# Optimization experiments

Measured on AMD Instinct MI355X. Metric: run time of the kernel, lower is better.

The kernel has to match this reference:

```python
import jax, jax.numpy as jnp
import numpy as np

IN_DIM = 256
INNER = IN_DIM // 8  # 32


def setup_inputs() -> dict:
    key = jax.random.key(0)
    ks = jax.random.split(key, 9)
    B, C, W, H = 4, IN_DIM, 64, 64
    sc = 0.05
    return {
        "x": jax.random.normal(ks[0], (B, C, W, H), dtype=jnp.float32),
        "Wf": jax.random.normal(ks[1], (INNER, C), dtype=jnp.float32) * sc,
        "bf": jnp.zeros((INNER,), dtype=jnp.float32),
        "Wg": jax.random.normal(ks[2], (INNER, C), dtype=jnp.float32) * sc,
        "bg": jnp.zeros((INNER,), dtype=jnp.float32),
        "Wh": jax.random.normal(ks[3], (INNER, C), dtype=jnp.float32) * sc,
        "bh": jnp.zeros((INNER,), dtype=jnp.float32),
        "Wv": jax.random.normal(ks[4], (C, INNER), dtype=jnp.float32) * sc,
        "bv": jnp.zeros((C,), dtype=jnp.float32),
        "gamma": jnp.ones((1,), dtype=jnp.float32) * 0.5,  # nonzero so attention path matters
    }


def reference(x, Wf, bf, Wg, bg, Wh, bh, Wv, bv, gamma):
    B, C, W, H = x.shape
    N = W * H
    xf = x.reshape(B, C, N)
    # 1x1 convs == per-pixel linear projections
    f = jnp.einsum('kc,bcn->bkn', Wf, xf) + bf[None, :, None]  # [B, C/8, N]
    g = jnp.einsum('kc,bcn->bkn', Wg, xf) + bg[None, :, None]
    h = jnp.einsum('kc,bcn->bkn', Wh, xf) + bh[None, :, None]
    # s[b,n,m] = sum_k f[b,k,n] * g[b,k,m]  (f^T @ g)
    s = jnp.einsum('bkn,bkm->bnm', f, g)                      # [B, N, N]
    attn = jax.nn.softmax(s, axis=-1)                          # softmax over last dim
    attn_map = jnp.transpose(attn, (0, 2, 1))                  # returned map (permuted)
    # o_pre = h_x @ attn_map : o_pre[b,k,m] = sum_n h[b,k,n] * attn[b,m,n]
    o_pre = jnp.einsum('bkn,bmn->bkm', h, attn)                # [B, C/8, N]
    o = jnp.einsum('ck,bkn->bcn', Wv, o_pre) + bv[None, :, None]
    o = o.reshape(B, C, W, H)
    y = gamma.reshape(()) * o + x
    return (y, attn_map)
```

## Files before the change

kernel.cpp:

```cpp
#include <hip/hip_runtime.h>
#include <cstddef>
#include <cstdint>

#define NB     4
#define CDIM   256
#define KD     32
#define NPIX   4096
#define SSHIFT 20.0f

typedef __attribute__((ext_vector_type(8))) short  bfrag;
typedef __attribute__((ext_vector_type(4))) float  facc;

#define MFMA(a,b,c) __builtin_amdgcn_mfma_f32_16x16x32_bf16((a),(b),(c),0,0,0)

__device__ __forceinline__ unsigned short f2bf(float x) {
    union { float f; unsigned u; } v; v.f = x;
    unsigned u = v.u + 0x7fffu + ((v.u >> 16) & 1u);
    return (unsigned short)(u >> 16);
}
__device__ __forceinline__ float bf2f(unsigned short h) {
    union { float f; unsigned u; } v; v.u = ((unsigned)h) << 16;
    return v.f;
}

#define OFF_FA_HI (0)
#define OFF_FA_LO (1u<<20)
#define OFF_GB_HI (2u<<20)
#define OFF_GB_LO (3u<<20)
#define OFF_HB    (4u<<20)
#define OFF_WA_HI (5u<<20)
#define OFF_WA_LO ((5u<<20) + 65536)
#define OFF_OT    ((5u<<20) + 131072)
#define OFF_RCP   ((5u<<20) + 131072 + (2u<<20))

__global__ __launch_bounds__(256) void wt_kernel(const float* __restrict__ Wf,
                                                 const float* __restrict__ Wg,
                                                 const float* __restrict__ Wh,
                                                 unsigned short* __restrict__ WA_hi,
                                                 unsigned short* __restrict__ WA_lo)
{
    int t = blockIdx.x * 256 + threadIdx.x;
    if (t >= 48 * 64) return;
    int tile = t >> 6, lane = t & 63;
    int rt = tile >> 3, cc = tile & 7;
    int q = lane >> 4, c15 = lane & 15;
    int row = rt * 16 + c15;
    const float* W = (row < 32) ? (Wf + (size_t)row * CDIM)
                   : (row < 64) ? (Wg + (size_t)(row - 32) * CDIM)
                                : (Wh + (size_t)(row - 64) * CDIM);
    int cb = cc * 32 + q * 8;
    bfrag vh, vl;
#pragma unroll
    for (int j = 0; j < 8; ++j) {
        float xv = W[cb + j];
        unsigned short h = f2bf(xv);
        vh[j] = (short)h;
        vl[j] = (short)f2bf(xv - bf2f(h));
    }
    *(bfrag*)(WA_hi + (size_t)t * 8) = vh;
    *(bfrag*)(WA_lo + (size_t)t * 8) = vl;
}

__global__ __launch_bounds__(256) void proj_kernel(const float* __restrict__ x,
                                                   const unsigned short* __restrict__ WA_hi,
                                                   const unsigned short* __restrict__ WA_lo,
                                                   const float* __restrict__ bfv,
                                                   const float* __restrict__ bgv,
                                                   const float* __restrict__ bhv,
                                                   unsigned short* __restrict__ fA_hi,
                                                   unsigned short* __restrict__ fA_lo,
                                                   unsigned short* __restrict__ gB_hi,
                                                   unsigned short* __restrict__ gB_lo,
                                                   unsigned short* __restrict__ hB)
{
    __shared__ float xs[32][65];
    __shared__ float os[96][65];
    __shared__ float bias_s[96];

    const int b  = blockIdx.y;
    const int n0 = blockIdx.x * 64;
    const int tid = threadIdx.x;
    const int w = tid >> 6, lane = tid & 63, q = lane >> 4, c15 = lane & 15;

    if (tid < 96)
        bias_s[tid] = (tid < 32) ? bfv[tid] : (tid < 64 ? bgv[tid - 32] : bhv[tid - 64]);

    facc acc[6];
#pragma unroll
    for (int rt = 0; rt < 6; ++rt) acc[rt] = (facc){0.f, 0.f, 0.f, 0.f};

    const float* xb = x + (size_t)b * CDIM * NPIX + n0;
    const int cr = tid >> 3, nb = (tid & 7) * 8;

    for (int cc = 0; cc < 8; ++cc) {
        const float* src = xb + (size_t)(cc * 32 + cr) * NPIX + nb;
        float4 va = *(const float4*)src;
        float4 vb = *(const float4*)(src + 4);
        __syncthreads();
        *(float4*)&xs[cr][nb]     = va;
        *(float4*)&xs[cr][nb + 4] = vb;
        __syncthreads();

        bfrag xh, xl;
#pragma unroll
        for (int j = 0; j < 8; ++j) {
            float xv = xs[q * 8 + j][w * 16 + c15];
            unsigned short h = f2bf(xv);
            xh[j] = (short)h;
            xl[j] = (short)f2bf(xv - bf2f(h));
        }
#pragma unroll
        for (int rt = 0; rt < 6; ++rt) {
            size_t wo = ((size_t)(rt * 8 + cc) * 64 + lane) * 8;
            bfrag wh = *(const bfrag*)(WA_hi + wo);
            bfrag wl = *(const bfrag*)(WA_lo + wo);
            acc[rt] = MFMA(wh, xh, acc[rt]);
            acc[rt] = MFMA(wh, xl, acc[rt]);
            acc[rt] = MFMA(wl, xh, acc[rt]);
        }
    }

#pragma unroll
    for (int rt = 0; rt < 6; ++rt)
#pragma unroll
        for (int i = 0; i < 4; ++i) {
            int row = rt * 16 + q * 4 + i;
            os[row][w * 16 + c15] = acc[rt][i] + bias_s[row];
        }
    __syncthreads();

    {
        bfrag vh, vl;
#pragma unroll
        for (int j = 0; j < 8; ++j) {
            float v = os[q * 8 + j][w * 16 + c15];
            unsigned short h = f2bf(v);
            vh[j] = (short)h; vl[j] = (short)f2bf(v - bf2f(h));
        }
        size_t o = ((size_t)(b * 256 + (n0 >> 4) + w) * 64 + lane) * 8;
        *(bfrag*)(fA_hi + o) = vh;
        *(bfrag*)(fA_lo + o) = vl;
#pragma unroll
        for (int j = 0; j < 8; ++j) {
            float v = os[32 + q * 8 + j][w * 16 + c15];
            unsigned short h = f2bf(v);
            vh[j] = (short)h; vl[j] = (short)f2bf(v - bf2f(h));
        }
        *(bfrag*)(gB_hi + o) = vh;
        *(bfrag*)(gB_lo + o) = vl;
        int mcl = w >> 1, kt = w & 1;
        bfrag hv;
#pragma unroll
        for (int j = 0; j < 8; ++j) {
            int p = q * 8 + j;
            int mp = (p & 1) * 16 + (p >> 1);
            float v = os[64 + kt * 16 + c15][mcl * 32 + mp];
            hv[j] = (short)f2bf(v);
        }
        size_t oh = ((size_t)((b * 128 + (n0 >> 5) + mcl) * 2 + kt) * 64 + lane) * 8;
        *(bfrag*)(hB + oh) = hv;
    }
}

__global__ __launch_bounds__(256) void attn_kernel(const unsigned short* __restrict__ fA_hi,
                                                   const unsigned short* __restrict__ fA_lo,
                                                   const unsigned short* __restrict__ gB_hi,
                                                   const unsigned short* __restrict__ gB_lo,
                                                   const unsigned short* __restrict__ hB,
                                                   float* __restrict__ rcp_g,
                                                   float* __restrict__ oT)
{
    __shared__ unsigned short Pst[4][16 * 40];
    __shared__ float red[4][64][8];
    __shared__ float sums_l[4][16];
    __shared__ float rcp_l[16];

    const int b  = blockIdx.y;
    const int r0 = blockIdx.x * 16;
    const int tid = threadIdx.x;
    const int w = tid >> 6, lane = tid & 63, q = lane >> 4, c15 = lane & 15;

    const size_t fo = ((size_t)(b * 256 + (r0 >> 4)) * 64 + lane) * 8;
    const bfrag fh = *(const bfrag*)(fA_hi + fo);
    const bfrag fl = *(const bfrag*)(fA_lo + fo);

    facc o0 = (facc){0.f,0.f,0.f,0.f}, o1 = (facc){0.f,0.f,0.f,0.f};
    float sum[4] = {0.f, 0.f, 0.f, 0.f};
    unsigned short* P = &Pst[w][0];

    const int ch0 = w * 32, ch1 = ch0 + 32;

    for (int mc = ch0; mc < ch1; ++mc) {
        size_t go = ((size_t)(b * 256 + 2 * mc) * 64 + lane) * 8;
        bfrag g0h = *(const bfrag*)(gB_hi + go);
        bfrag g1h = *(const bfrag*)(gB_hi + go + 512);
        bfrag g0l = *(const bfrag*)(gB_lo + go);
        bfrag g1l = *(const bfrag*)(gB_lo + go + 512);
        size_t ho = ((size_t)(b * 128 + mc) * 2 * 64 + lane) * 8;
        bfrag h0 = *(const bfrag*)(hB + ho);
        bfrag h1 = *(const bfrag*)(hB + ho + 512);

        facc s0 = (facc){0.f,0.f,0.f,0.f}, s1 = (facc){0.f,0.f,0.f,0.f};
        s0 = MFMA(fh, g0h, s0); s0 = MFMA(fh, g0l, s0); s0 = MFMA(fl, g0h, s0);
        s1 = MFMA(fh, g1h, s1); s1 = MFMA(fh, g1l, s1); s1 = MFMA(fl, g1h, s1);

        float e0[4], e1[4];
#pragma unroll
        for (int i = 0; i < 4; ++i) {
            e0[i] = __expf(s0[i] - SSHIFT);
            e1[i] = __expf(s1[i] - SSHIFT);
            sum[i] += e0[i] + e1[i];
        }
#pragma unroll
        for (int i = 0; i < 4; ++i) {
            unsigned pr = (unsigned)f2bf(e0[i]) | ((unsigned)f2bf(e1[i]) << 16);
            *(unsigned*)&P[(4 * q + i) * 40 + 2 * c15] = pr;
        }
        bfrag pA = *(const bfrag*)&P[c15 * 40 + q * 8];
        o0 = MFMA(pA, h0, o0);
        o1 = MFMA(pA, h1, o1);
    }

#pragma unroll
    for (int m = 1; m < 16; m <<= 1)
#pragma unroll
        for (int i = 0; i < 4; ++i) sum[i] += __shfl_xor(sum[i], m);
    if (c15 == 0) {
#pragma unroll
        for (int i = 0; i < 4; ++i) sums_l[w][4 * q + i] = sum[i];
    }
    *(facc*)&red[w][lane][0] = o0;
    *(facc*)&red[w][lane][4] = o1;
    __syncthreads();
    if (tid < 16) {
        float rv = 1.0f / (sums_l[0][tid] + sums_l[1][tid] + sums_l[2][tid] + sums_l[3][tid]);
        rcp_l[tid] = rv;
        rcp_g[(size_t)b * NPIX + r0 + tid] = rv;
    }
    __syncthreads();

    if (w == 0) {
        facc a = (facc){0.f,0.f,0.f,0.f}, bb = (facc){0.f,0.f,0.f,0.f};
#pragma unroll
        for (int ww = 0; ww < 4; ++ww) {
            a  += *(const facc*)&red[ww][lane][0];
            bb += *(const facc*)&red[ww][lane][4];
        }
#pragma unroll
        for (int i = 0; i < 4; ++i) {
            int r = 4 * q + i;
            float rc = rcp_l[r];
            oT[((size_t)(b * NPIX + r0 + r)) * KD + c15]      = a[i] * rc;
            oT[((size_t)(b * NPIX + r0 + r)) * KD + 16 + c15] = bb[i] * rc;
        }
    }
}

__global__ __launch_bounds__(256) void attn2_kernel(const unsigned short* __restrict__ fA_hi,
                                                    const unsigned short* __restrict__ fA_lo,
                                                    const unsigned short* __restrict__ gB_hi,
                                                    const unsigned short* __restrict__ gB_lo,
                                                    const float* __restrict__ rcp_g,
                                                    float* __restrict__ am)
{
    const int b   = blockIdx.y;
    const int mt  = blockIdx.x;
    const int tid = threadIdx.x;
    const int w = tid >> 6, lane = tid & 63, q = lane >> 4, c15 = lane & 15;

    const size_t ga = ((size_t)(b * 256 + mt) * 64 + lane) * 8;
    const bfrag a_hi = *(const bfrag*)(gB_hi + ga);
    const bfrag a_lo = *(const bfrag*)(gB_lo + ga);

    const int m0 = mt * 16 + q * 4;
    float* amrow = am + (size_t)b * NPIX * NPIX + (size_t)m0 * NPIX;
    const float* rcp_b = rcp_g + (size_t)b * NPIX;

#pragma unroll 2
    for (int t = 0; t < 64; ++t) {
        const int nt = w * 64 + t;
        const size_t fo = ((size_t)(b * 256 + nt) * 64 + lane) * 8;
        bfrag b_hi = *(const bfrag*)(fA_hi + fo);
        bfrag b_lo = *(const bfrag*)(fA_lo + fo);

        facc s = (facc){0.f,0.f,0.f,0.f};
        s = MFMA(a_hi, b_hi, s);
        s = MFMA(a_hi, b_lo, s);
        s = MFMA(a_lo, b_hi, s);

        const int n = nt * 16 + c15;
        const float rc = rcp_b[n];
#pragma unroll
        for (int i = 0; i < 4; ++i)
            amrow[(size_t)i * NPIX + n] = __expf(s[i] - SSHIFT) * rc;
    }
}

__global__ __launch_bounds__(256) void out_kernel(const float* __restrict__ x,
                                                  const float* __restrict__ oT,
                                                  const float* __restrict__ Wv,
                                                  const float* __restrict__ bv,
                                                  const float* __restrict__ gamma,
                                                  float* __restrict__ y)
{
    __shared__ float wv_s[CDIM * KD];
    const int b  = blockIdx.y;
    const int tid = threadIdx.x;
    const int n = blockIdx.x * 64 + (tid & 63);
    const int cg = tid >> 6;

    for (int i = tid * 4; i < CDIM * KD; i += 1024)
        *(float4*)&wv_s[i] = *(const float4*)&Wv[i];

    float op[KD];
    {
        const float4* src = (const float4*)&oT[((size_t)(b * NPIX + n)) * KD];
#pragma unroll
        for (int qq = 0; qq < 8; ++qq) {
            float4 v = src[qq];
            op[qq * 4 + 0] = v.x; op[qq * 4 + 1] = v.y;
            op[qq * 4 + 2] = v.z; op[qq * 4 + 3] = v.w;
        }
    }
    __syncthreads();
    const float gm = gamma[0];

    for (int c = cg * 64; c < cg * 64 + 64; ++c) {
        float a = 0.f;
#pragma unroll
        for (int k4 = 0; k4 < 8; ++k4) {
            float4 wv4 = *(const float4*)&wv_s[c * KD + k4 * 4];
            a = fmaf(wv4.x, op[k4 * 4 + 0], a);
            a = fmaf(wv4.y, op[k4 * 4 + 1], a);
            a = fmaf(wv4.z, op[k4 * 4 + 2], a);
            a = fmaf(wv4.w, op[k4 * 4 + 3], a);
        }
        size_t idx = ((size_t)(b * CDIM + c)) * NPIX + n;
        y[idx] = fmaf(gm, a + bv[c], x[idx]);
    }
}

extern "C" void kernel_launch(void* const* d_in, const int* in_sizes, int n_in,
                              void* d_out, int out_size, void* d_ws, size_t ws_size,
                              hipStream_t stream)
{
    const float* x     = (const float*)d_in[0];
    const float* Wf    = (const float*)d_in[1];
    const float* bfv   = (const float*)d_in[2];
    const float* Wg    = (const float*)d_in[3];
    const float* bgv   = (const float*)d_in[4];
    const float* Wh    = (const float*)d_in[5];
    const float* bhv   = (const float*)d_in[6];
    const float* Wv    = (const float*)d_in[7];
    const float* bv    = (const float*)d_in[8];
    const float* gamma = (const float*)d_in[9];

    char* ws = (char*)d_ws;
    unsigned short* fA_hi = (unsigned short*)(ws + OFF_FA_HI);
    unsigned short* fA_lo = (unsigned short*)(ws + OFF_FA_LO);
    unsigned short* gB_hi = (unsigned short*)(ws + OFF_GB_HI);
    unsigned short* gB_lo = (unsigned short*)(ws + OFF_GB_LO);
    unsigned short* hB    = (unsigned short*)(ws + OFF_HB);
    unsigned short* WA_hi = (unsigned short*)(ws + OFF_WA_HI);
    unsigned short* WA_lo = (unsigned short*)(ws + OFF_WA_LO);
    float*          oT    = (float*)(ws + OFF_OT);
    float*          rcp_g = (float*)(ws + OFF_RCP);

    float* y  = (float*)d_out;
    float* am = (float*)d_out + (size_t)NB * CDIM * NPIX;

    hipLaunchKernelGGL(wt_kernel, dim3(12), dim3(256), 0, stream, Wf, Wg, Wh, WA_hi, WA_lo);
    hipLaunchKernelGGL(proj_kernel, dim3(NPIX / 64, NB), dim3(256), 0, stream,
                       x, WA_hi, WA_lo, bfv, bgv, bhv, fA_hi, fA_lo, gB_hi, gB_lo, hB);
    hipLaunchKernelGGL(attn_kernel, dim3(NPIX / 16, NB), dim3(256), 0, stream,
                       fA_hi, fA_lo, gB_hi, gB_lo, hB, rcp_g, oT);
    hipLaunchKernelGGL(attn2_kernel, dim3(NPIX / 16, NB), dim3(256), 0, stream,
                       fA_hi, fA_lo, gB_hi, gB_lo, rcp_g, am);
    hipLaunchKernelGGL(out_kernel, dim3(NPIX / 64, NB), dim3(256), 0, stream,
                       x, oT, Wv, bv, gamma, y);
}
```

Baseline: 412.3 us.

## Merge attention-map and output kernels into one launch with nontemporal stores

Combines the attention-map writer and the output projection into a single tail kernel, with blocks dispatched by blockIdx.x to one role or the other, so the two independent stages overlap and one launch is saved. Each attention-map block now handles two 16-row m tiles, reusing every loaded f fragment for both. The large attention-map and y writes use nontemporal stores to avoid polluting the cache. In exchange every block reserves the 32KB shared buffer even when only the output blocks use it, which can lower occupancy for the attention-map blocks, and halving their count may reduce parallelism.

```diff
diff --git a/kernel.cpp b/kernel.cpp
--- a/kernel.cpp
+++ b/kernel.cpp
@@ -256,87 +256,97 @@
     }
 }
 
-__global__ __launch_bounds__(256) void attn2_kernel(const unsigned short* __restrict__ fA_hi,
-                                                    const unsigned short* __restrict__ fA_lo,
-                                                    const unsigned short* __restrict__ gB_hi,
-                                                    const unsigned short* __restrict__ gB_lo,
-                                                    const float* __restrict__ rcp_g,
-                                                    float* __restrict__ am)
-{
+__global__ __launch_bounds__(256) void tail_kernel(const unsigned short* __restrict__ fA_hi,
+                                                   const unsigned short* __restrict__ fA_lo,
+                                                   const unsigned short* __restrict__ gB_hi,
+                                                   const unsigned short* __restrict__ gB_lo,
+                                                   const float* __restrict__ rcp_g,
+                                                   float* __restrict__ am,
+                                                   const float* __restrict__ x,
+                                                   const float* __restrict__ oT,
+                                                   const float* __restrict__ Wv,
+                                                   const float* __restrict__ bv,
+                                                   const float* __restrict__ gamma,
+                                                   float* __restrict__ y)
+{
+    __shared__ float wv_s[CDIM * KD];
+
     const int b   = blockIdx.y;
-    const int mt  = blockIdx.x;
+    const int bx  = blockIdx.x;
     const int tid = threadIdx.x;
-    const int w = tid >> 6, lane = tid & 63, q = lane >> 4, c15 = lane & 15;
-
-    const size_t ga = ((size_t)(b * 256 + mt) * 64 + lane) * 8;
-    const bfrag a_hi = *(const bfrag*)(gB_hi + ga);
-    const bfrag a_lo = *(const bfrag*)(gB_lo + ga);
-
-    const int m0 = mt * 16 + q * 4;
-    float* amrow = am + (size_t)b * NPIX * NPIX + (size_t)m0 * NPIX;
-    const float* rcp_b = rcp_g + (size_t)b * NPIX;
+
+    if (bx < 128) {
+        const int w = tid >> 6, lane = tid & 63, q = lane >> 4, c15 = lane & 15;
+
+        const size_t ga = ((size_t)(b * 256 + 2 * bx) * 64 + lane) * 8;
+        const bfrag a0h = *(const bfrag*)(gB_hi + ga);
+        const bfrag a0l = *(const bfrag*)(gB_lo + ga);
+        const bfrag a1h = *(const bfrag*)(gB_hi + ga + 512);
+        const bfrag a1l = *(const bfrag*)(gB_lo + ga + 512);
+
+        const int m0 = bx * 32 + q * 4;
+        float* amrow = am + (size_t)b * NPIX * NPIX + (size_t)m0 * NPIX;
+        const float* rcp_b = rcp_g + (size_t)b * NPIX;
 
 #pragma unroll 2
-    for (int t = 0; t < 64; ++t) {
-        const int nt = w * 64 + t;
-        const size_t fo = ((size_t)(b * 256 + nt) * 64 + lane) * 8;
-        bfrag b_hi = *(const bfrag*)(fA_hi + fo);
-        bfrag b_lo = *(const bfrag*)(fA_lo + fo);
-
-        facc s = (facc){0.f,0.f,0.f,0.f};
-        s = MFMA(a_hi, b_hi, s);
-        s = MFMA(a_hi, b_lo, s);
-        s = MFMA(a_lo, b_hi, s);
-
-        const int n = nt * 16 + c15;
-        const float rc = rcp_b[n];
-#pragma unroll
-        for (int i = 0; i < 4; ++i)
-            amrow[(size_t)i * NPIX + n] = __expf(s[i] - SSHIFT) * rc;
-    }
-}
-
-__global__ __launch_bounds__(256) void out_kernel(const float* __restrict__ x,
-                                                  const float* __restrict__ oT,
-                                                  const float* __restrict__ Wv,
-                                                  const float* __restrict__ bv,
-                                                  const float* __restrict__ gamma,
-                                                  float* __restrict__ y)
-{
-    __shared__ float wv_s[CDIM * KD];
-    const int b  = blockIdx.y;
-    const int tid = threadIdx.x;
-    const int n = blockIdx.x * 64 + (tid & 63);
-    const int cg = tid >> 6;
-
-    for (int i = tid * 4; i < CDIM * KD; i += 1024)
-        *(float4*)&wv_s[i] = *(const float4*)&Wv[i];
-
-    float op[KD];
-    {
-        const float4* src = (const float4*)&oT[((size_t)(b * NPIX + n)) * KD];
-#pragma unroll
-        for (int qq = 0; qq < 8; ++qq) {
-            float4 v = src[qq];
-            op[qq * 4 + 0] = v.x; op[qq * 4 + 1] = v.y;
-            op[qq * 4 + 2] = v.z; op[qq * 4 + 3] = v.w;
-        }
-    }
-    __syncthreads();
-    const float gm = gamma[0];
-
-    for (int c = cg * 64; c < cg * 64 + 64; ++c) {
-        float a = 0.f;
-#pragma unroll
-        for (int k4 = 0; k4 < 8; ++k4) {
-            float4 wv4 = *(const float4*)&wv_s[c * KD + k4 * 4];
-            a = fmaf(wv4.x, op[k4 * 4 + 0], a);
-            a = fmaf(wv4.y, op[k4 * 4 + 1], a);
-            a = fmaf(wv4.z, op[k4 * 4 + 2], a);
-            a = fmaf(wv4.w, op[k4 * 4 + 3], a);
-        }
-        size_t idx = ((size_t)(b * CDIM + c)) * NPIX + n;
-        y[idx] = fmaf(gm, a + bv[c], x[idx]);
+        for (int t = 0; t < 64; ++t) {
+            const int nt = w * 64 + t;
+            const size_t fo = ((size_t)(b * 256 + nt) * 64 + lane) * 8;
+            bfrag b_hi = *(const bfrag*)(fA_hi + fo);
+            bfrag b_lo = *(const bfrag*)(fA_lo + fo);
+
+            facc s0 = (facc){0.f,0.f,0.f,0.f};
+            s0 = MFMA(a0h, b_hi, s0);
+            s0 = MFMA(a0h, b_lo, s0);
+            s0 = MFMA(a0l, b_hi, s0);
+            facc s1 = (facc){0.f,0.f,0.f,0.f};
+            s1 = MFMA(a1h, b_hi, s1);
+            s1 = MFMA(a1h, b_lo, s1);
+            s1 = MFMA(a1l, b_hi, s1);
+
+            const int n = nt * 16 + c15;
+            const float rc = rcp_b[n];
+#pragma unroll
+            for (int i = 0; i < 4; ++i) {
+                __builtin_nontemporal_store(__expf(s0[i] - SSHIFT) * rc,
+                                            &amrow[(size_t)i * NPIX + n]);
+                __builtin_nontemporal_store(__expf(s1[i] - SSHIFT) * rc,
+                                            &amrow[(size_t)(16 + i) * NPIX + n]);
+            }
+        }
+    } else {
+        const int n = (bx - 128) * 64 + (tid & 63);
+        const int cg = tid >> 6;
+
+        for (int i = tid * 4; i < CDIM * KD; i += 1024)
+            *(float4*)&wv_s[i] = *(const float4*)&Wv[i];
+
+        float op[KD];
+        {
+            const float4* src = (const float4*)&oT[((size_t)(b * NPIX + n)) * KD];
+#pragma unroll
+            for (int qq = 0; qq < 8; ++qq) {
+                float4 v = src[qq];
+                op[qq * 4 + 0] = v.x; op[qq * 4 + 1] = v.y;
+                op[qq * 4 + 2] = v.z; op[qq * 4 + 3] = v.w;
+            }
+        }
+        __syncthreads();
+        const float gm = gamma[0];
+
+        for (int c = cg * 64; c < cg * 64 + 64; ++c) {
+            float a = 0.f;
+#pragma unroll
+            for (int k4 = 0; k4 < 8; ++k4) {
+                float4 wv4 = *(const float4*)&wv_s[c * KD + k4 * 4];
+                a = fmaf(wv4.x, op[k4 * 4 + 0], a);
+                a = fmaf(wv4.y, op[k4 * 4 + 1], a);
+                a = fmaf(wv4.z, op[k4 * 4 + 2], a);
+                a = fmaf(wv4.w, op[k4 * 4 + 3], a);
+            }
+            size_t idx = ((size_t)(b * CDIM + c)) * NPIX + n;
+            __builtin_nontemporal_store(fmaf(gm, a + bv[c], x[idx]), &y[idx]);
+        }
     }
 }
 
@@ -374,8 +384,6 @@
                        x, WA_hi, WA_lo, bfv, bgv, bhv, fA_hi, fA_lo, gB_hi, gB_lo, hB);
     hipLaunchKernelGGL(attn_kernel, dim3(NPIX / 16, NB), dim3(256), 0, stream,
                        fA_hi, fA_lo, gB_hi, gB_lo, hB, rcp_g, oT);
-    hipLaunchKernelGGL(attn2_kernel, dim3(NPIX / 16, NB), dim3(256), 0, stream,
-                       fA_hi, fA_lo, gB_hi, gB_lo, rcp_g, am);
-    hipLaunchKernelGGL(out_kernel, dim3(NPIX / 64, NB), dim3(256), 0, stream,
-                       x, oT, Wv, bv, gamma, y);
-}
+    hipLaunchKernelGGL(tail_kernel, dim3(128 + NPIX / 64, NB), dim3(256), 0, stream,
+                       fA_hi, fA_lo, gB_hi, gB_lo, rcp_g, am, x, oT, Wv, bv, gamma, y);
+}
```

Result: slower. 428.8 us (+4.0%).

## Fuse pipeline into cooperative persistent kernel and fold output projection into attention

Applied to the files above, without the earlier changes.

Merges the weight prep, projection, attention and attention-map stages into one cooperative kernel with grid-wide syncs, which removes several kernel launches. The output 1x1 conv and residual are folded into the attention kernel through a shared-memory oT tile, so the global oT buffer and its round trip go away. Attention-map writes now use nontemporal stores. In exchange, the large shared allocation in the mega kernel limits occupancy, the grid syncs add barrier cost, and if the cooperative launch fails the code falls back to separate kernels.

```diff
diff --git a/kernel.cpp b/kernel.cpp
--- a/kernel.cpp
+++ b/kernel.cpp
@@ -1,6 +1,9 @@
 #include <hip/hip_runtime.h>
+#include <hip/hip_cooperative_groups.h>
 #include <cstddef>
 #include <cstdint>
+
+namespace cg = cooperative_groups;
 
 #define NB     4
 #define CDIM   256
@@ -30,17 +33,24 @@
 #define OFF_HB    (4u<<20)
 #define OFF_WA_HI (5u<<20)
 #define OFF_WA_LO ((5u<<20) + 65536)
-#define OFF_OT    ((5u<<20) + 131072)
 #define OFF_RCP   ((5u<<20) + 131072 + (2u<<20))
 
-__global__ __launch_bounds__(256) void wt_kernel(const float* __restrict__ Wf,
-                                                 const float* __restrict__ Wg,
-                                                 const float* __restrict__ Wh,
-                                                 unsigned short* __restrict__ WA_hi,
-                                                 unsigned short* __restrict__ WA_lo)
-{
-    int t = blockIdx.x * 256 + threadIdx.x;
-    if (t >= 48 * 64) return;
+#define SM_PROJ_BYTES 33664
+#define SM_XS   0
+#define SM_OS   8320
+#define SM_BIAS 33280
+#define SM_PST  0
+#define SM_RED  5120
+#define SM_SUMS 13312
+#define SM_RCPL 13568
+#define SM_OTS  13632
+#define SM_ATTN_BYTES 15680
+
+__device__ __forceinline__ void wt_body(int t,
+        const float* __restrict__ Wf, const float* __restrict__ Wg,
+        const float* __restrict__ Wh,
+        unsigned short* __restrict__ WA_hi, unsigned short* __restrict__ WA_lo)
+{
     int tile = t >> 6, lane = t & 63;
     int rt = tile >> 3, cc = tile & 7;
     int q = lane >> 4, c15 = lane & 15;
@@ -61,25 +71,19 @@
     *(bfrag*)(WA_lo + (size_t)t * 8) = vl;
 }
 
-__global__ __launch_bounds__(256) void proj_kernel(const float* __restrict__ x,
-                                                   const unsigned short* __restrict__ WA_hi,
-                                                   const unsigned short* __restrict__ WA_lo,
-                                                   const float* __restrict__ bfv,
-                                                   const float* __restrict__ bgv,
-                                                   const float* __restrict__ bhv,
-                                                   unsigned short* __restrict__ fA_hi,
-                                                   unsigned short* __restrict__ fA_lo,
-                                                   unsigned short* __restrict__ gB_hi,
-                                                   unsigned short* __restrict__ gB_lo,
-                                                   unsigned short* __restrict__ hB)
-{
-    __shared__ float xs[32][65];
-    __shared__ float os[96][65];
-    __shared__ float bias_s[96];
-
-    const int b  = blockIdx.y;
-    const int n0 = blockIdx.x * 64;
-    const int tid = threadIdx.x;
+__device__ __forceinline__ void proj_body(char* smem, int b, int n0, int tid,
+        const float* __restrict__ x,
+        const unsigned short* __restrict__ WA_hi, const unsigned short* __restrict__ WA_lo,
+        const float* __restrict__ bfv, const float* __restrict__ bgv,
+        const float* __restrict__ bhv,
+        unsigned short* __restrict__ fA_hi, unsigned short* __restrict__ fA_lo,
+        unsigned short* __restrict__ gB_hi, unsigned short* __restrict__ gB_lo,
+        unsigned short* __restrict__ hB)
+{
+    float* xs     = (float*)(smem + SM_XS);
+    float* os     = (float*)(smem + SM_OS);
+    float* bias_s = (float*)(smem + SM_BIAS);
+
     const int w = tid >> 6, lane = tid & 63, q = lane >> 4, c15 = lane & 15;
 
     if (tid < 96)
@@ -97,14 +101,14 @@
         float4 va = *(const float4*)src;
         float4 vb = *(const float4*)(src + 4);
         __syncthreads();
-        *(float4*)&xs[cr][nb]     = va;
-        *(float4*)&xs[cr][nb + 4] = vb;
+        *(float4*)&xs[cr * 65 + nb]     = va;
+        *(float4*)&xs[cr * 65 + nb + 4] = vb;
         __syncthreads();
 
         bfrag xh, xl;
 #pragma unroll
         for (int j = 0; j < 8; ++j) {
-            float xv = xs[q * 8 + j][w * 16 + c15];
+            float xv = xs[(q * 8 + j) * 65 + w * 16 + c15];
             unsigned short h = f2bf(xv);
             xh[j] = (short)h;
             xl[j] = (short)f2bf(xv - bf2f(h));
@@ -125,7 +129,7 @@
 #pragma unroll
         for (int i = 0; i < 4; ++i) {
             int row = rt * 16 + q * 4 + i;
-            os[row][w * 16 + c15] = acc[rt][i] + bias_s[row];
+            os[row * 65 + w * 16 + c15] = acc[rt][i] + bias_s[row];
         }
     __syncthreads();
 
@@ -133,7 +137,7 @@
         bfrag vh, vl;
 #pragma unroll
         for (int j = 0; j < 8; ++j) {
-            float v = os[q * 8 + j][w * 16 + c15];
+            float v = os[(q * 8 + j) * 65 + w * 16 + c15];
             unsigned short h = f2bf(v);
             vh[j] = (short)h; vl[j] = (short)f2bf(v - bf2f(h));
         }
@@ -142,7 +146,7 @@
         *(bfrag*)(fA_lo + o) = vl;
 #pragma unroll
         for (int j = 0; j < 8; ++j) {
-            float v = os[32 + q * 8 + j][w * 16 + c15];
+            float v = os[(32 + q * 8 + j) * 65 + w * 16 + c15];
             unsigned short h = f2bf(v);
             vh[j] = (short)h; vl[j] = (short)f2bf(v - bf2f(h));
         }
@@ -154,7 +158,7 @@
         for (int j = 0; j < 8; ++j) {
             int p = q * 8 + j;
             int mp = (p & 1) * 16 + (p >> 1);
-            float v = os[64 + kt * 16 + c15][mcl * 32 + mp];
+            float v = os[(64 + kt * 16 + c15) * 65 + mcl * 32 + mp];
             hv[j] = (short)f2bf(v);
         }
         size_t oh = ((size_t)((b * 128 + (n0 >> 5) + mcl) * 2 + kt) * 64 + lane) * 8;
@@ -162,22 +166,20 @@
     }
 }
 
-__global__ __launch_bounds__(256) void attn_kernel(const unsigned short* __restrict__ fA_hi,
-                                                   const unsigned short* __restrict__ fA_lo,
-                                                   const unsigned short* __restrict__ gB_hi,
-                                                   const unsigned short* __restrict__ gB_lo,
-                                                   const unsigned short* __restrict__ hB,
-                                                   float* __restrict__ rcp_g,
-                                                   float* __restrict__ oT)
-{
-    __shared__ unsigned short Pst[4][16 * 40];
-    __shared__ float red[4][64][8];
-    __shared__ float sums_l[4][16];
-    __shared__ float rcp_l[16];
-
-    const int b  = blockIdx.y;
-    const int r0 = blockIdx.x * 16;
-    const int tid = threadIdx.x;
+__device__ __forceinline__ void attn1_body(char* smem, int b, int r0, int tid,
+        const unsigned short* __restrict__ fA_hi, const unsigned short* __restrict__ fA_lo,
+        const unsigned short* __restrict__ gB_hi, const unsigned short* __restrict__ gB_lo,
+        const unsigned short* __restrict__ hB, float* __restrict__ rcp_g,
+        const float* __restrict__ x, const float* __restrict__ Wv,
+        const float* __restrict__ bv, const float* __restrict__ gamma,
+        float* __restrict__ y)
+{
+    unsigned short* Pst = (unsigned short*)(smem + SM_PST);
+    float* red    = (float*)(smem + SM_RED);
+    float* sums_l = (float*)(smem + SM_SUMS);
+    float* rcp_l  = (float*)(smem + SM_RCPL);
+    float* oTs    = (float*)(smem + SM_OTS);
+
     const int w = tid >> 6, lane = tid & 63, q = lane >> 4, c15 = lane & 15;
 
     const size_t fo = ((size_t)(b * 256 + (r0 >> 4)) * 64 + lane) * 8;
@@ -186,7 +188,7 @@
 
     facc o0 = (facc){0.f,0.f,0.f,0.f}, o1 = (facc){0.f,0.f,0.f,0.f};
     float sum[4] = {0.f, 0.f, 0.f, 0.f};
-    unsigned short* P = &Pst[w][0];
+    unsigned short* P = Pst + w * 640;
 
     const int ch0 = w * 32, ch1 = ch0 + 32;
 
@@ -227,13 +229,13 @@
         for (int i = 0; i < 4; ++i) sum[i] += __shfl_xor(sum[i], m);
     if (c15 == 0) {
 #pragma unroll
-        for (int i = 0; i < 4; ++i) sums_l[w][4 * q + i] = sum[i];
-    }
-    *(facc*)&red[w][lane][0] = o0;
-    *(facc*)&red[w][lane][4] = o1;
+        for (int i = 0; i < 4; ++i) sums_l[w * 16 + 4 * q + i] = sum[i];
+    }
+    *(facc*)&red[(w * 64 + lane) * 8]     = o0;
+    *(facc*)&red[(w * 64 + lane) * 8 + 4] = o1;
     __syncthreads();
     if (tid < 16) {
-        float rv = 1.0f / (sums_l[0][tid] + sums_l[1][tid] + sums_l[2][tid] + sums_l[3][tid]);
+        float rv = 1.0f / (sums_l[tid] + sums_l[16 + tid] + sums_l[32 + tid] + sums_l[48 + tid]);
         rcp_l[tid] = rv;
         rcp_g[(size_t)b * NPIX + r0 + tid] = rv;
     }
@@ -243,29 +245,56 @@
         facc a = (facc){0.f,0.f,0.f,0.f}, bb = (facc){0.f,0.f,0.f,0.f};
 #pragma unroll
         for (int ww = 0; ww < 4; ++ww) {
-            a  += *(const facc*)&red[ww][lane][0];
-            bb += *(const facc*)&red[ww][lane][4];
+            a  += *(const facc*)&red[(ww * 64 + lane) * 8];
+            bb += *(const facc*)&red[(ww * 64 + lane) * 8 + 4];
         }
 #pragma unroll
         for (int i = 0; i < 4; ++i) {
             int r = 4 * q + i;
             float rc = rcp_l[r];
-            oT[((size_t)(b * NPIX + r0 + r)) * KD + c15]      = a[i] * rc;
-            oT[((size_t)(b * NPIX + r0 + r)) * KD + 16 + c15] = bb[i] * rc;
-        }
-    }
-}
-
-__global__ __launch_bounds__(256) void attn2_kernel(const unsigned short* __restrict__ fA_hi,
-                                                    const unsigned short* __restrict__ fA_lo,
-                                                    const unsigned short* __restrict__ gB_hi,
-                                                    const unsigned short* __restrict__ gB_lo,
-                                                    const float* __restrict__ rcp_g,
-                                                    float* __restrict__ am)
-{
-    const int b   = blockIdx.y;
-    const int mt  = blockIdx.x;
-    const int tid = threadIdx.x;
+            oTs[r * 32 + c15]      = a[i] * rc;
+            oTs[r * 32 + 16 + c15] = bb[i] * rc;
+        }
+    }
+    __syncthreads();
+
+    {
+        const int c = w * 64 + lane;
+        const float gm = gamma[0];
+        const float4* wvp = (const float4*)(Wv + (size_t)c * KD);
+        float4 wv[8];
+#pragma unroll
+        for (int k4 = 0; k4 < 8; ++k4) wv[k4] = wvp[k4];
+        const float bvc = bv[c];
+        const size_t base = ((size_t)(b * CDIM + c)) * NPIX + r0;
+#pragma unroll
+        for (int nn = 0; nn < 16; nn += 4) {
+            float4 xv = *(const float4*)(x + base + nn);
+            float4 yo;
+#pragma unroll
+            for (int j = 0; j < 4; ++j) {
+                const float4* ot = (const float4*)(oTs + (nn + j) * 32);
+                float a = 0.f;
+#pragma unroll
+                for (int k4 = 0; k4 < 8; ++k4) {
+                    float4 o4 = ot[k4];
+                    a = fmaf(wv[k4].x, o4.x, a);
+                    a = fmaf(wv[k4].y, o4.y, a);
+                    a = fmaf(wv[k4].z, o4.z, a);
+                    a = fmaf(wv[k4].w, o4.w, a);
+                }
+                ((float*)&yo)[j] = fmaf(gm, a + bvc, ((float*)&xv)[j]);
+            }
+            *(float4*)(y + base + nn) = yo;
+        }
+    }
+}
+
+__device__ __forceinline__ void attn2_body(int b, int mt, int tid,
+        const unsigned short* __restrict__ fA_hi, const unsigned short* __restrict__ fA_lo,
+        const unsigned short* __restrict__ gB_hi, const unsigned short* __restrict__ gB_lo,
+        const float* __restrict__ rcp_g, float* __restrict__ am)
+{
     const int w = tid >> 6, lane = tid & 63, q = lane >> 4, c15 = lane & 15;
 
     const size_t ga = ((size_t)(b * 256 + mt) * 64 + lane) * 8;
@@ -292,52 +321,91 @@
         const float rc = rcp_b[n];
 #pragma unroll
         for (int i = 0; i < 4; ++i)
-            amrow[(size_t)i * NPIX + n] = __expf(s[i] - SSHIFT) * rc;
-    }
-}
-
-__global__ __launch_bounds__(256) void out_kernel(const float* __restrict__ x,
-                                                  const float* __restrict__ oT,
-                                                  const float* __restrict__ Wv,
-                                                  const float* __restrict__ bv,
-                                                  const float* __restrict__ gamma,
-                                                  float* __restrict__ y)
-{
-    __shared__ float wv_s[CDIM * KD];
-    const int b  = blockIdx.y;
+            __builtin_nontemporal_store(__expf(s[i] - SSHIFT) * rc,
+                                        &amrow[(size_t)i * NPIX + n]);
+    }
+}
+
+__global__ __launch_bounds__(256, 4) void mega_kernel(
+        const float* __restrict__ x,
+        const float* __restrict__ Wf, const float* __restrict__ bfv,
+        const float* __restrict__ Wg, const float* __restrict__ bgv,
+        const float* __restrict__ Wh, const float* __restrict__ bhv,
+        const float* __restrict__ Wv, const float* __restrict__ bv,
+        const float* __restrict__ gamma,
+        unsigned short* __restrict__ fA_hi, unsigned short* __restrict__ fA_lo,
+        unsigned short* __restrict__ gB_hi, unsigned short* __restrict__ gB_lo,
+        unsigned short* __restrict__ hB,
+        unsigned short* __restrict__ WA_hi, unsigned short* __restrict__ WA_lo,
+        float* __restrict__ rcp_g, float* __restrict__ am, float* __restrict__ y)
+{
+    cg::grid_group grid = cg::this_grid();
+    __shared__ __align__(16) char smem[SM_PROJ_BYTES];
+
+    const int gid = blockIdx.x;
     const int tid = threadIdx.x;
-    const int n = blockIdx.x * 64 + (tid & 63);
-    const int cg = tid >> 6;
-
-    for (int i = tid * 4; i < CDIM * KD; i += 1024)
-        *(float4*)&wv_s[i] = *(const float4*)&Wv[i];
-
-    float op[KD];
-    {
-        const float4* src = (const float4*)&oT[((size_t)(b * NPIX + n)) * KD];
-#pragma unroll
-        for (int qq = 0; qq < 8; ++qq) {
-            float4 v = src[qq];
-            op[qq * 4 + 0] = v.x; op[qq * 4 + 1] = v.y;
-            op[qq * 4 + 2] = v.z; op[qq * 4 + 3] = v.w;
-        }
-    }
-    __syncthreads();
-    const float gm = gamma[0];
-
-    for (int c = cg * 64; c < cg * 64 + 64; ++c) {
-        float a = 0.f;
-#pragma unroll
-        for (int k4 = 0; k4 < 8; ++k4) {
-            float4 wv4 = *(const float4*)&wv_s[c * KD + k4 * 4];
-            a = fmaf(wv4.x, op[k4 * 4 + 0], a);
-            a = fmaf(wv4.y, op[k4 * 4 + 1], a);
-            a = fmaf(wv4.z, op[k4 * 4 + 2], a);
-            a = fmaf(wv4.w, op[k4 * 4 + 3], a);
-        }
-        size_t idx = ((size_t)(b * CDIM + c)) * NPIX + n;
-        y[idx] = fmaf(gm, a + bv[c], x[idx]);
-    }
+
+    if (gid < 12) {
+        int t = gid * 256 + tid;
+        if (t < 48 * 64)
+            wt_body(t, Wf, Wg, Wh, WA_hi, WA_lo);
+    }
+    grid.sync();
+
+    if (gid < 256)
+        proj_body(smem, gid >> 6, (gid & 63) * 64, tid,
+                  x, WA_hi, WA_lo, bfv, bgv, bhv, fA_hi, fA_lo, gB_hi, gB_lo, hB);
+    grid.sync();
+
+    attn1_body(smem, gid >> 8, (gid & 255) * 16, tid,
+               fA_hi, fA_lo, gB_hi, gB_lo, hB, rcp_g, x, Wv, bv, gamma, y);
+    grid.sync();
+
+    attn2_body(gid >> 8, gid & 255, tid, fA_hi, fA_lo, gB_hi, gB_lo, rcp_g, am);
+}
+
+__global__ __launch_bounds__(256) void wt_kernel(const float* __restrict__ Wf,
+                                                 const float* __restrict__ Wg,
+                                                 const float* __restrict__ Wh,
+                                                 unsigned short* __restrict__ WA_hi,
+                                                 unsigned short* __restrict__ WA_lo)
+{
+    int t = blockIdx.x * 256 + threadIdx.x;
+    if (t < 48 * 64) wt_body(t, Wf, Wg, Wh, WA_hi, WA_lo);
+}
+
+__global__ __launch_bounds__(256) void proj_kernel(const float* __restrict__ x,
+        const unsigned short* __restrict__ WA_hi, const unsigned short* __restrict__ WA_lo,
+        const float* __restrict__ bfv, const float* __restrict__ bgv,
+        const float* __restrict__ bhv,
+        unsigned short* __restrict__ fA_hi, unsigned short* __restrict__ fA_lo,
+        unsigned short* __restrict__ gB_hi, unsigned short* __restrict__ gB_lo,
+        unsigned short* __restrict__ hB)
+{
+    __shared__ __align__(16) char smem[SM_PROJ_BYTES];
+    proj_body(smem, blockIdx.y, blockIdx.x * 64, threadIdx.x,
+              x, WA_hi, WA_lo, bfv, bgv, bhv, fA_hi, fA_lo, gB_hi, gB_lo, hB);
+}
+
+__global__ __launch_bounds__(256) void attn1_kernel(
+        const unsigned short* __restrict__ fA_hi, const unsigned short* __restrict__ fA_lo,
+        const unsigned short* __restrict__ gB_hi, const unsigned short* __restrict__ gB_lo,
+        const unsigned short* __restrict__ hB, float* __restrict__ rcp_g,
+        const float* __restrict__ x, const float* __restrict__ Wv,
+        const float* __restrict__ bv, const float* __restrict__ gamma,
+        float* __restrict__ y)
+{
+    __shared__ __align__(16) char smem[SM_ATTN_BYTES];
+    attn1_body(smem, blockIdx.y, blockIdx.x * 16, threadIdx.x,
+               fA_hi, fA_lo, gB_hi, gB_lo, hB, rcp_g, x, Wv, bv, gamma, y);
+}
+
+__global__ __launch_bounds__(256) void attn2_kernel(
+        const unsigned short* __restrict__ fA_hi, const unsigned short* __restrict__ fA_lo,
+        const unsigned short* __restrict__ gB_hi, const unsigned short* __restrict__ gB_lo,
+        const float* __restrict__ rcp_g, float* __restrict__ am)
+{
+    attn2_body(blockIdx.y, blockIdx.x, threadIdx.x, fA_hi, fA_lo, gB_hi, gB_lo, rcp_g, am);
 }
 
 extern "C" void kernel_launch(void* const* d_in, const int* in_sizes, int n_in,
@@ -363,19 +431,26 @@
     unsigned short* hB    = (unsigned short*)(ws + OFF_HB);
     unsigned short* WA_hi = (unsigned short*)(ws + OFF_WA_HI);
     unsigned short* WA_lo = (unsigned short*)(ws + OFF_WA_LO);
-    float*          oT    = (float*)(ws + OFF_OT);
     float*          rcp_g = (float*)(ws + OFF_RCP);
 
     float* y  = (float*)d_out;
     float* am = (float*)d_out + (size_t)NB * CDIM * NPIX;
 
-    hipLaunchKernelGGL(wt_kernel, dim3(12), dim3(256), 0, stream, Wf, Wg, Wh, WA_hi, WA_lo);
-    hipLaunchKernelGGL(proj_kernel, dim3(NPIX / 64, NB), dim3(256), 0, stream,
-                       x, WA_hi, WA_lo, bfv, bgv, bhv, fA_hi, fA_lo, gB_hi, gB_lo, hB);
-    hipLaunchKernelGGL(attn_kernel, dim3(NPIX / 16, NB), dim3(256), 0, stream,
-                       fA_hi, fA_lo, gB_hi, gB_lo, hB, rcp_g, oT);
-    hipLaunchKernelGGL(attn2_kernel, dim3(NPIX / 16, NB), dim3(256), 0, stream,
-                       fA_hi, fA_lo, gB_hi, gB_lo, rcp_g, am);
-    hipLaunchKernelGGL(out_kernel, dim3(NPIX / 64, NB), dim3(256), 0, stream,
-                       x, oT, Wv, bv, gamma, y);
-}
+    void* args[] = { &x, &Wf, &bfv, &Wg, &bgv, &Wh, &bhv, &Wv, &bv, &gamma,
+                     &fA_hi, &fA_lo, &gB_hi, &gB_lo, &hB, &WA_hi, &WA_lo,
+                     &rcp_g, &am, &y };
+    hipError_t e = hipLaunchCooperativeKernel(
+        reinterpret_cast<const void*>(&mega_kernel),
+        dim3(1024), dim3(256), args, 0u, stream);
+
+    if (e != hipSuccess) {
+        hipLaunchKernelGGL(wt_kernel, dim3(12), dim3(256), 0, stream,
+                           Wf, Wg, Wh, WA_hi, WA_lo);
+        hipLaunchKernelGGL(proj_kernel, dim3(NPIX / 64, NB), dim3(256), 0, stream,
+                           x, WA_hi, WA_lo, bfv, bgv, bhv, fA_hi, fA_lo, gB_hi, gB_lo, hB);
+        hipLaunchKernelGGL(attn1_kernel, dim3(NPIX / 16, NB), dim3(256), 0, stream,
+                           fA_hi, fA_lo, gB_hi, gB_lo, hB, rcp_g, x, Wv, bv, gamma, y);
+        hipLaunchKernelGGL(attn2_kernel, dim3(NPIX / 16, NB), dim3(256), 0, stream,
+                           fA_hi, fA_lo, gB_hi, gB_lo, rcp_g, am);
+    }
+}
```

New measurement: 691.8 us. 67.8% more time.

## Prefetch next-iteration fragments and remap blocks for XCD-local batch placement

Applied to the files above, without the earlier changes.

Both attention kernels now load the next iteration's g/h (or f) fragments and the reciprocal before computing the current step, a software-pipelining step meant to hide global load latency behind MFMA and exp work. The grids are flattened to 1D, and block ids are remapped so that consecutive ids, which are dealt round-robin across the 8 XCDs, land so that each XCD works on a single batch. This keeps that batch's g/h/f data in one XCD's L2. The cost is extra registers for the prefetched fragments, which may lower occupancy.

```diff
diff --git a/kernel.cpp b/kernel.cpp
--- a/kernel.cpp
+++ b/kernel.cpp
@@ -162,6 +162,28 @@
     }
 }
 
+#define ATTN1_STEP(G0H,G1H,G0L,G1L,H0,H1)                                       \
+    {                                                                           \
+        facc s0 = (facc){0.f,0.f,0.f,0.f}, s1 = (facc){0.f,0.f,0.f,0.f};        \
+        s0 = MFMA(fh, G0H, s0); s0 = MFMA(fh, G0L, s0); s0 = MFMA(fl, G0H, s0); \
+        s1 = MFMA(fh, G1H, s1); s1 = MFMA(fh, G1L, s1); s1 = MFMA(fl, G1H, s1); \
+        float e0[4], e1[4];                                                     \
+        _Pragma("unroll")                                                       \
+        for (int i = 0; i < 4; ++i) {                                           \
+            e0[i] = __expf(s0[i] - SSHIFT);                                     \
+            e1[i] = __expf(s1[i] - SSHIFT);                                     \
+            sum[i] += e0[i] + e1[i];                                            \
+        }                                                                       \
+        _Pragma("unroll")                                                       \
+        for (int i = 0; i < 4; ++i) {                                           \
+            unsigned pr = (unsigned)f2bf(e0[i]) | ((unsigned)f2bf(e1[i]) << 16);\
+            *(unsigned*)&P[(4 * q + i) * 40 + 2 * c15] = pr;                    \
+        }                                                                       \
+        bfrag pA = *(const bfrag*)&P[c15 * 40 + q * 8];                         \
+        o0 = MFMA(pA, H0, o0);                                                  \
+        o1 = MFMA(pA, H1, o1);                                                  \
+    }
+
 __global__ __launch_bounds__(256) void attn_kernel(const unsigned short* __restrict__ fA_hi,
                                                    const unsigned short* __restrict__ fA_lo,
                                                    const unsigned short* __restrict__ gB_hi,
@@ -175,8 +197,10 @@
     __shared__ float sums_l[4][16];
     __shared__ float rcp_l[16];
 
-    const int b  = blockIdx.y;
-    const int r0 = blockIdx.x * 16;
+    const int bid = blockIdx.x;
+    const int xcd = bid & 7, jj = bid >> 3;
+    const int b  = xcd >> 1;
+    const int r0 = ((xcd & 1) * 128 + jj) * 16;
     const int tid = threadIdx.x;
     const int w = tid >> 6, lane = tid & 63, q = lane >> 4, c15 = lane & 15;
 
@@ -190,36 +214,27 @@
 
     const int ch0 = w * 32, ch1 = ch0 + 32;
 
-    for (int mc = ch0; mc < ch1; ++mc) {
-        size_t go = ((size_t)(b * 256 + 2 * mc) * 64 + lane) * 8;
-        bfrag g0h = *(const bfrag*)(gB_hi + go);
-        bfrag g1h = *(const bfrag*)(gB_hi + go + 512);
-        bfrag g0l = *(const bfrag*)(gB_lo + go);
-        bfrag g1l = *(const bfrag*)(gB_lo + go + 512);
-        size_t ho = ((size_t)(b * 128 + mc) * 2 * 64 + lane) * 8;
-        bfrag h0 = *(const bfrag*)(hB + ho);
-        bfrag h1 = *(const bfrag*)(hB + ho + 512);
-
-        facc s0 = (facc){0.f,0.f,0.f,0.f}, s1 = (facc){0.f,0.f,0.f,0.f};
-        s0 = MFMA(fh, g0h, s0); s0 = MFMA(fh, g0l, s0); s0 = MFMA(fl, g0h, s0);
-        s1 = MFMA(fh, g1h, s1); s1 = MFMA(fh, g1l, s1); s1 = MFMA(fl, g1h, s1);
-
-        float e0[4], e1[4];
-#pragma unroll
-        for (int i = 0; i < 4; ++i) {
-            e0[i] = __expf(s0[i] - SSHIFT);
-            e1[i] = __expf(s1[i] - SSHIFT);
-            sum[i] += e0[i] + e1[i];
-        }
-#pragma unroll
-        for (int i = 0; i < 4; ++i) {
-            unsigned pr = (unsigned)f2bf(e0[i]) | ((unsigned)f2bf(e1[i]) << 16);
-            *(unsigned*)&P[(4 * q + i) * 40 + 2 * c15] = pr;
-        }
-        bfrag pA = *(const bfrag*)&P[c15 * 40 + q * 8];
-        o0 = MFMA(pA, h0, o0);
-        o1 = MFMA(pA, h1, o1);
-    }
+    size_t go = ((size_t)(b * 256 + 2 * ch0) * 64 + lane) * 8;
+    size_t ho = ((size_t)((b * 128 + ch0) * 2) * 64 + lane) * 8;
+    bfrag g0h = *(const bfrag*)(gB_hi + go);
+    bfrag g1h = *(const bfrag*)(gB_hi + go + 512);
+    bfrag g0l = *(const bfrag*)(gB_lo + go);
+    bfrag g1l = *(const bfrag*)(gB_lo + go + 512);
+    bfrag h0  = *(const bfrag*)(hB + ho);
+    bfrag h1  = *(const bfrag*)(hB + ho + 512);
+
+    for (int mc = ch0; mc < ch1 - 1; ++mc) {
+        go += 1024; ho += 1024;
+        bfrag ng0h = *(const bfrag*)(gB_hi + go);
+        bfrag ng1h = *(const bfrag*)(gB_hi + go + 512);
+        bfrag ng0l = *(const bfrag*)(gB_lo + go);
+        bfrag ng1l = *(const bfrag*)(gB_lo + go + 512);
+        bfrag nh0  = *(const bfrag*)(hB + ho);
+        bfrag nh1  = *(const bfrag*)(hB + ho + 512);
+        ATTN1_STEP(g0h, g1h, g0l, g1l, h0, h1);
+        g0h = ng0h; g1h = ng1h; g0l = ng0l; g1l = ng1l; h0 = nh0; h1 = nh1;
+    }
+    ATTN1_STEP(g0h, g1h, g0l, g1l, h0, h1);
 
 #pragma unroll
     for (int m = 1; m < 16; m <<= 1)
@@ -256,6 +271,17 @@
     }
 }
 
+#define ATTN2_STEP(BH,BL,RC,N)                                                  \
+    {                                                                           \
+        facc s = (facc){0.f,0.f,0.f,0.f};                                       \
+        s = MFMA(a_hi, BH, s);                                                  \
+        s = MFMA(a_hi, BL, s);                                                  \
+        s = MFMA(a_lo, BH, s);                                                  \
+        _Pragma("unroll")                                                       \
+        for (int i = 0; i < 4; ++i)                                             \
+            amrow[(size_t)i * NPIX + (N)] = __expf(s[i] - SSHIFT) * (RC);       \
+    }
+
 __global__ __launch_bounds__(256) void attn2_kernel(const unsigned short* __restrict__ fA_hi,
                                                     const unsigned short* __restrict__ fA_lo,
                                                     const unsigned short* __restrict__ gB_hi,
@@ -263,8 +289,10 @@
                                                     const float* __restrict__ rcp_g,
                                                     float* __restrict__ am)
 {
-    const int b   = blockIdx.y;
-    const int mt  = blockIdx.x;
+    const int bid = blockIdx.x;
+    const int xcd = bid & 7, jj = bid >> 3;
+    const int b  = xcd >> 1;
+    const int mt = (xcd & 1) * 128 + jj;
     const int tid = threadIdx.x;
     const int w = tid >> 6, lane = tid & 63, q = lane >> 4, c15 = lane & 15;
 
@@ -276,24 +304,21 @@
     float* amrow = am + (size_t)b * NPIX * NPIX + (size_t)m0 * NPIX;
     const float* rcp_b = rcp_g + (size_t)b * NPIX;
 
-#pragma unroll 2
-    for (int t = 0; t < 64; ++t) {
-        const int nt = w * 64 + t;
-        const size_t fo = ((size_t)(b * 256 + nt) * 64 + lane) * 8;
-        bfrag b_hi = *(const bfrag*)(fA_hi + fo);
-        bfrag b_lo = *(const bfrag*)(fA_lo + fo);
-
-        facc s = (facc){0.f,0.f,0.f,0.f};
-        s = MFMA(a_hi, b_hi, s);
-        s = MFMA(a_hi, b_lo, s);
-        s = MFMA(a_lo, b_hi, s);
-
-        const int n = nt * 16 + c15;
-        const float rc = rcp_b[n];
-#pragma unroll
-        for (int i = 0; i < 4; ++i)
-            amrow[(size_t)i * NPIX + n] = __expf(s[i] - SSHIFT) * rc;
-    }
+    size_t fo = ((size_t)(b * 256 + w * 64) * 64 + lane) * 8;
+    int n = (w * 64) * 16 + c15;
+    bfrag bh = *(const bfrag*)(fA_hi + fo);
+    bfrag bl = *(const bfrag*)(fA_lo + fo);
+    float rc = rcp_b[n];
+
+    for (int t = 0; t < 63; ++t) {
+        fo += 512;
+        bfrag nbh = *(const bfrag*)(fA_hi + fo);
+        bfrag nbl = *(const bfrag*)(fA_lo + fo);
+        float nrc = rcp_b[n + 16];
+        ATTN2_STEP(bh, bl, rc, n);
+        bh = nbh; bl = nbl; rc = nrc; n += 16;
+    }
+    ATTN2_STEP(bh, bl, rc, n);
 }
 
 __global__ __launch_bounds__(256) void out_kernel(const float* __restrict__ x,
@@ -372,9 +397,9 @@
     hipLaunchKernelGGL(wt_kernel, dim3(12), dim3(256), 0, stream, Wf, Wg, Wh, WA_hi, WA_lo);
     hipLaunchKernelGGL(proj_kernel, dim3(NPIX / 64, NB), dim3(256), 0, stream,
                        x, WA_hi, WA_lo, bfv, bgv, bhv, fA_hi, fA_lo, gB_hi, gB_lo, hB);
-    hipLaunchKernelGGL(attn_kernel, dim3(NPIX / 16, NB), dim3(256), 0, stream,
+    hipLaunchKernelGGL(attn_kernel, dim3(1024), dim3(256), 0, stream,
                        fA_hi, fA_lo, gB_hi, gB_lo, hB, rcp_g, oT);
-    hipLaunchKernelGGL(attn2_kernel, dim3(NPIX / 16, NB), dim3(256), 0, stream,
+    hipLaunchKernelGGL(attn2_kernel, dim3(1024), dim3(256), 0, stream,
                        fA_hi, fA_lo, gB_hi, gB_lo, rcp_g, am);
     hipLaunchKernelGGL(out_kernel, dim3(NPIX / 64, NB), dim3(256), 0, stream,
                        x, oT, Wv, bv, gamma, y);
```

After: 424.8 us. 1.03x slower.
